# Kernel tuning notes

Hardware: AMD Instinct MI355X
Metric: run time of the kernel (lower is better)

## Reference

```python
import jax, jax.numpy as jnp
import numpy as np

UNITS = 128
D_FEAT = 128
B, N = 4, 4096
EDGE_PROB = 0.01  # avg in-degree ~ N * EDGE_PROB ~ 41


def setup_inputs() -> dict:
    key = jax.random.key(0)
    k1, k2, k3, k4 = jax.random.split(key, 4)
    x = jax.random.normal(k1, (B, N, D_FEAT), dtype=jnp.float32)
    # binary adjacency mask, as consumed by tf.where(adj)
    adj = (jax.random.uniform(k2, (B, N, N)) < EDGE_PROB).astype(jnp.float32)
    # Dense(units, use_bias=False) kernels: msg on concat(x_snd, x_rec) -> [2d, U];
    # node_update on concat(x, messages) -> [d+U, U]
    W_msg = (jax.random.normal(k3, (2 * D_FEAT, UNITS), dtype=jnp.float32)
             / np.sqrt(2 * D_FEAT).astype(np.float32))
    W_upd = (jax.random.normal(k4, (D_FEAT + UNITS, UNITS), dtype=jnp.float32)
             / np.sqrt(D_FEAT + UNITS).astype(np.float32))
    return {"x": x, "adj": adj, "W_msg": W_msg, "W_upd": W_upd}


def reference(x, adj, W_msg, W_upd):
    # Faithful to MPNN2.call: edges are (b, s, r) where adj[b, s, r] != 0.
    # message per edge = concat(x[b,s], x[b,r]) @ W_msg = x[b,s]@Ws + x[b,r]@Wr.
    # messages[b,r] = segment_mean over incoming edges. Since the receiver term
    # x[b,r]@Wr is identical for all edges into r, its mean is itself, and the
    # sender term's mean is (adj^T @ (x@Ws)) / in_degree. Empty segments -> 0
    # (tf.math.unsorted_segment_mean semantics). This avoids data-dependent
    # edge-list shapes and is jit-compatible.
    d = x.shape[-1]
    Ws, Wr = W_msg[:d], W_msg[d:]          # [d, U] each
    xs = x @ Ws                            # sender contribution  [B, N, U]
    xr = x @ Wr                            # receiver contribution [B, N, U]
    deg = jnp.einsum('bsr->br', adj)[..., None]          # in-degree [B, N, 1]
    snd_sum = jnp.einsum('bsr,bsu->bru', adj, xs)        # [B, N, U]
    messages = jnp.where(deg > 0,
                         snd_sum / jnp.maximum(deg, 1.0) + xr,
                         0.0)
    # node_update on concat(x, messages); activation=None, use_bias=False
    return jnp.concatenate([x, messages], axis=-1) @ W_upd
```

## Files before the change

kernel.cpp:

```cpp
#include <hip/hip_runtime.h>
#include <hip/hip_bf16.h>

#define BB 4
#define NN 4096
#define ROWS (BB*NN)
#define RT 128
#define SC 512
#define NCH (NN/SC)
#define CAPC 32
#define BSTRIDE (NCH*CAPC)

typedef __attribute__((ext_vector_type(8))) short short8;
typedef __attribute__((ext_vector_type(4))) float f32x4;

__device__ __forceinline__ float asf(unsigned int u) {
    union { unsigned int i; float f; } cv; cv.i = u; return cv.f;
}
__device__ __forceinline__ unsigned short f2bf(float f) {
    union { float f; unsigned int i; } cv; cv.f = f;
    unsigned int i = cv.i;
    return (unsigned short)((i + 0x7FFFu + ((i >> 16) & 1u)) >> 16);
}

__global__ __launch_bounds__(256) void scan_bucket(const float* __restrict__ adj,
                                                   int* __restrict__ cnt2,
                                                   int* __restrict__ bucket) {
    __shared__ int lcnt[RT];
    int bI = blockIdx.x;
    int rt = bI & 31;
    int ch = (bI >> 5) & 7;
    int b  = bI >> 8;
    int r0 = rt * RT;
    int s0 = ch * SC;
    int t  = threadIdx.x;
    if (t < RT) lcnt[t] = 0;
    __syncthreads();
    int cg = t & 31;
    int sl = t >> 5;
    const float* base = adj + ((size_t)b * NN + s0) * NN + r0 + cg * 4;
    for (int k = 0; k < SC / 32; ++k) {
        float4 v[4];
#pragma unroll
        for (int u = 0; u < 4; ++u)
            v[u] = *(const float4*)(base + (size_t)(k * 32 + u * 8 + sl) * NN);
#pragma unroll
        for (int u = 0; u < 4; ++u) {
            int s = s0 + k * 32 + u * 8 + sl;
            float vals[4] = {v[u].x, v[u].y, v[u].z, v[u].w};
#pragma unroll
            for (int j = 0; j < 4; ++j) {
                if (vals[j] != 0.0f) {
                    int col = cg * 4 + j;
                    int slot = atomicAdd(&lcnt[col], 1);
                    if (slot < CAPC)
                        bucket[(size_t)((b << 12) + r0 + col) * BSTRIDE + ch * CAPC + slot] = s;
                }
            }
        }
    }
    __syncthreads();
    if (t < RT) cnt2[(size_t)((b << 12) + r0 + t) * NCH + ch] = lcnt[t];
}

__global__ __launch_bounds__(128) void fold_weights(const float* __restrict__ Wmsg,
                                                    const float* __restrict__ Wupd,
                                                    unsigned short* __restrict__ WcatT) {
    __shared__ float ldsS[128], ldsR[128];
    int k = blockIdx.x, t = threadIdx.x;
    ldsS[t] = Wmsg[k * 128 + t];
    ldsR[t] = Wmsg[(128 + k) * 128 + t];
    __syncthreads();
    float a1 = 0.f, a2 = 0.f;
#pragma unroll 8
    for (int m = 0; m < 128; ++m) {
        float wu = Wupd[(128 + m) * 128 + t];
        a1 += ldsS[m] * wu;
        a2 += ldsR[m] * wu;
    }
    WcatT[(size_t)t * 128 + k]         = f2bf(Wupd[k * 128 + t]);
    WcatT[(size_t)(128 + t) * 128 + k] = f2bf(a2);
    WcatT[(size_t)(256 + t) * 128 + k] = f2bf(a1);
}

__global__ __launch_bounds__(256) void gemm_mfma(const float* __restrict__ X,
                                                 const unsigned short* __restrict__ WcatT,
                                                 float* __restrict__ TD,
                                                 unsigned short* __restrict__ YB) {
    __shared__ unsigned short Al[64][136];
    __shared__ unsigned short Bl[128][136];
    int t  = threadIdx.x;
    int m0 = blockIdx.x * 64;
    int nb = blockIdx.y;

    {
        int m = t >> 2, seg = t & 3;
        const float* src = X + (size_t)(m0 + m) * 128 + seg * 32;
#pragma unroll
        for (int i = 0; i < 8; ++i) {
            float4 v = *(const float4*)(src + i * 4);
            ushort4 p;
            p.x = f2bf(v.x); p.y = f2bf(v.y); p.z = f2bf(v.z); p.w = f2bf(v.w);
            *(ushort4*)&Al[m][seg * 32 + i * 4] = p;
        }
    }
    {
        int n = t >> 1, half = t & 1;
        const unsigned short* src = WcatT + (size_t)(nb * 128 + n) * 128 + half * 64;
#pragma unroll
        for (int i = 0; i < 8; ++i) {
            uint4 v = *(const uint4*)(src + i * 8);
            *(uint4*)&Bl[n][half * 64 + i * 8] = v;
        }
    }
    __syncthreads();

    int lane = t & 63, wave = t >> 6;
    int quad = lane >> 4, lr = lane & 15;
    int wm = wave * 16;
    f32x4 acc[8];
#pragma unroll
    for (int s = 0; s < 8; ++s) acc[s] = (f32x4)0.f;

#pragma unroll
    for (int kk = 0; kk < 4; ++kk) {
        short8 a = *(short8*)&Al[wm + lr][kk * 32 + quad * 8];
#pragma unroll
        for (int s = 0; s < 8; ++s) {
            short8 bf = *(short8*)&Bl[s * 16 + lr][kk * 32 + quad * 8];
            acc[s] = __builtin_amdgcn_mfma_f32_16x16x32_bf16(a, bf, acc[s], 0, 0, 0);
        }
    }

    if (nb == 2) {
#pragma unroll
        for (int s = 0; s < 8; ++s)
#pragma unroll
            for (int r = 0; r < 4; ++r) {
                int row = m0 + wm + quad * 4 + r;
                YB[(size_t)row * 128 + s * 16 + lr] = f2bf(acc[s][r]);
            }
    } else {
#pragma unroll
        for (int s = 0; s < 8; ++s)
#pragma unroll
            for (int r = 0; r < 4; ++r) {
                int row = m0 + wm + quad * 4 + r;
                TD[(size_t)row * 256 + nb * 128 + s * 16 + lr] = acc[s][r];
            }
    }
}

__global__ __launch_bounds__(256) void gather_out(const float* __restrict__ TD,
                                                  const unsigned int* __restrict__ YB,
                                                  const int* __restrict__ cnt2,
                                                  const int* __restrict__ bucket,
                                                  float* __restrict__ out) {
    __shared__ int lds_s[4][BSTRIDE];
    int t  = threadIdx.x;
    int rs = t >> 6;
    int j2 = t & 63;
    int rg = blockIdx.x * 4 + rs;

    int c[NCH];
    int ctot = 0, deg = 0;
    int pre[NCH];
#pragma unroll
    for (int ch = 0; ch < NCH; ++ch) {
        c[ch] = cnt2[(size_t)rg * NCH + ch];
        deg += c[ch];
        int cc = min(c[ch], CAPC);
        pre[ch] = ctot;
        ctot += cc;
    }
#pragma unroll
    for (int ch = 0; ch < NCH; ++ch) {
        int cc = min(c[ch], CAPC);
        if (j2 < cc)
            lds_s[rs][pre[ch] + j2] = bucket[(size_t)rg * BSTRIDE + ch * CAPC + j2];
    }
    __syncthreads();

    const float2* td = (const float2*)(TD + (size_t)rg * 256);
    float2 t1 = td[j2];
    float2 res = t1;
    if (deg > 0) {
        int b = rg >> 12;
        const unsigned int* yb = YB + (((size_t)b << 12)) * 64 + j2;
        float al0 = 0.f, ah0 = 0.f, al1 = 0.f, ah1 = 0.f;
        float al2 = 0.f, ah2 = 0.f, al3 = 0.f, ah3 = 0.f;
        int e = 0;
        for (; e + 4 <= ctot; e += 4) {
            int s0 = lds_s[rs][e + 0];
            int s1 = lds_s[rs][e + 1];
            int s2 = lds_s[rs][e + 2];
            int s3 = lds_s[rs][e + 3];
            unsigned u0 = yb[(size_t)s0 * 64];
            unsigned u1 = yb[(size_t)s1 * 64];
            unsigned u2 = yb[(size_t)s2 * 64];
            unsigned u3 = yb[(size_t)s3 * 64];
            al0 += asf(u0 << 16); ah0 += asf(u0 & 0xffff0000u);
            al1 += asf(u1 << 16); ah1 += asf(u1 & 0xffff0000u);
            al2 += asf(u2 << 16); ah2 += asf(u2 & 0xffff0000u);
            al3 += asf(u3 << 16); ah3 += asf(u3 & 0xffff0000u);
        }
        for (; e < ctot; ++e) {
            unsigned u = yb[(size_t)lds_s[rs][e] * 64];
            al0 += asf(u << 16); ah0 += asf(u & 0xffff0000u);
        }
        float inv = 1.0f / (float)deg;
        float2 d2 = td[64 + j2];
        res.x = t1.x + d2.x + (al0 + al1 + al2 + al3) * inv;
        res.y = t1.y + d2.y + (ah0 + ah1 + ah2 + ah3) * inv;
    }
    ((float2*)(out + (size_t)rg * 128))[j2] = res;
}

extern "C" void kernel_launch(void* const* d_in, const int* in_sizes, int n_in,
                              void* d_out, int out_size, void* d_ws, size_t ws_size,
                              hipStream_t stream) {
    const float* x    = (const float*)d_in[0];
    const float* adj  = (const float*)d_in[1];
    const float* Wmsg = (const float*)d_in[2];
    const float* Wupd = (const float*)d_in[3];
    float* out = (float*)d_out;

    char* ws = (char*)d_ws;
    unsigned short* WcatT  = (unsigned short*)(ws);
    float*          TD     = (float*)(ws + 131072);
    unsigned short* YB     = (unsigned short*)(ws + 131072 + 16777216);
    int*            cnt2   = (int*)(ws + 131072 + 16777216 + 4194304);
    int*            bucket = (int*)(ws + 131072 + 16777216 + 4194304 + 524288);

    scan_bucket<<<1024, 256, 0, stream>>>(adj, cnt2, bucket);
    fold_weights<<<128, 128, 0, stream>>>(Wmsg, Wupd, WcatT);
    gemm_mfma<<<dim3(256, 3), 256, 0, stream>>>(x, WcatT, TD, YB);
    gather_out<<<ROWS / 4, 256, 0, stream>>>(TD, (const unsigned int*)YB, cnt2, bucket, out);
}
```

Measured before the change: 433.2 us.

## Replace sparse bucket scan and gather with dense bf16 MFMA SpMM over adjacency

```diff
diff --git a/kernel.cpp b/kernel.cpp
--- a/kernel.cpp
+++ b/kernel.cpp
@@ -4,62 +4,14 @@
 #define BB 4
 #define NN 4096
 #define ROWS (BB*NN)
-#define RT 128
-#define SC 512
-#define NCH (NN/SC)
-#define CAPC 32
-#define BSTRIDE (NCH*CAPC)
 
 typedef __attribute__((ext_vector_type(8))) short short8;
 typedef __attribute__((ext_vector_type(4))) float f32x4;
 
-__device__ __forceinline__ float asf(unsigned int u) {
-    union { unsigned int i; float f; } cv; cv.i = u; return cv.f;
-}
 __device__ __forceinline__ unsigned short f2bf(float f) {
     union { float f; unsigned int i; } cv; cv.f = f;
     unsigned int i = cv.i;
     return (unsigned short)((i + 0x7FFFu + ((i >> 16) & 1u)) >> 16);
-}
-
-__global__ __launch_bounds__(256) void scan_bucket(const float* __restrict__ adj,
-                                                   int* __restrict__ cnt2,
-                                                   int* __restrict__ bucket) {
-    __shared__ int lcnt[RT];
-    int bI = blockIdx.x;
-    int rt = bI & 31;
-    int ch = (bI >> 5) & 7;
-    int b  = bI >> 8;
-    int r0 = rt * RT;
-    int s0 = ch * SC;
-    int t  = threadIdx.x;
-    if (t < RT) lcnt[t] = 0;
-    __syncthreads();
-    int cg = t & 31;
-    int sl = t >> 5;
-    const float* base = adj + ((size_t)b * NN + s0) * NN + r0 + cg * 4;
-    for (int k = 0; k < SC / 32; ++k) {
-        float4 v[4];
-#pragma unroll
-        for (int u = 0; u < 4; ++u)
-            v[u] = *(const float4*)(base + (size_t)(k * 32 + u * 8 + sl) * NN);
-#pragma unroll
-        for (int u = 0; u < 4; ++u) {
-            int s = s0 + k * 32 + u * 8 + sl;
-            float vals[4] = {v[u].x, v[u].y, v[u].z, v[u].w};
-#pragma unroll
-            for (int j = 0; j < 4; ++j) {
-                if (vals[j] != 0.0f) {
-                    int col = cg * 4 + j;
-                    int slot = atomicAdd(&lcnt[col], 1);
-                    if (slot < CAPC)
-                        bucket[(size_t)((b << 12) + r0 + col) * BSTRIDE + ch * CAPC + slot] = s;
-                }
-            }
-        }
-    }
-    __syncthreads();
-    if (t < RT) cnt2[(size_t)((b << 12) + r0 + t) * NCH + ch] = lcnt[t];
 }
 
 __global__ __launch_bounds__(128) void fold_weights(const float* __restrict__ Wmsg,
@@ -85,7 +37,7 @@
 __global__ __launch_bounds__(256) void gemm_mfma(const float* __restrict__ X,
                                                  const unsigned short* __restrict__ WcatT,
                                                  float* __restrict__ TD,
-                                                 unsigned short* __restrict__ YB) {
+                                                 unsigned short* __restrict__ YT) {
     __shared__ unsigned short Al[64][136];
     __shared__ unsigned short Bl[128][136];
     int t  = threadIdx.x;
@@ -132,13 +84,16 @@
     }
 
     if (nb == 2) {
-#pragma unroll
-        for (int s = 0; s < 8; ++s)
-#pragma unroll
-            for (int r = 0; r < 4; ++r) {
-                int row = m0 + wm + quad * 4 + r;
-                YB[(size_t)row * 128 + s * 16 + lr] = f2bf(acc[s][r]);
-            }
+        int row0 = m0 + wm + quad * 4;
+        int b = row0 >> 12, s0 = row0 & 4095;
+#pragma unroll
+        for (int s = 0; s < 8; ++s) {
+            int u = s * 16 + lr;
+            ushort4 pk;
+            pk.x = f2bf(acc[s][0]); pk.y = f2bf(acc[s][1]);
+            pk.z = f2bf(acc[s][2]); pk.w = f2bf(acc[s][3]);
+            *(ushort4*)(&YT[((size_t)b * 128 + u) * 4096 + s0]) = pk;
+        }
     } else {
 #pragma unroll
         for (int s = 0; s < 8; ++s)
@@ -150,69 +105,86 @@
     }
 }
 
-__global__ __launch_bounds__(256) void gather_out(const float* __restrict__ TD,
-                                                  const unsigned int* __restrict__ YB,
-                                                  const int* __restrict__ cnt2,
-                                                  const int* __restrict__ bucket,
-                                                  float* __restrict__ out) {
-    __shared__ int lds_s[4][BSTRIDE];
-    int t  = threadIdx.x;
-    int rs = t >> 6;
-    int j2 = t & 63;
-    int rg = blockIdx.x * 4 + rs;
-
-    int c[NCH];
-    int ctot = 0, deg = 0;
-    int pre[NCH];
-#pragma unroll
-    for (int ch = 0; ch < NCH; ++ch) {
-        c[ch] = cnt2[(size_t)rg * NCH + ch];
-        deg += c[ch];
-        int cc = min(c[ch], CAPC);
-        pre[ch] = ctot;
-        ctot += cc;
-    }
-#pragma unroll
-    for (int ch = 0; ch < NCH; ++ch) {
-        int cc = min(c[ch], CAPC);
-        if (j2 < cc)
-            lds_s[rs][pre[ch] + j2] = bucket[(size_t)rg * BSTRIDE + ch * CAPC + j2];
-    }
-    __syncthreads();
-
-    const float2* td = (const float2*)(TD + (size_t)rg * 256);
-    float2 t1 = td[j2];
-    float2 res = t1;
-    if (deg > 0) {
-        int b = rg >> 12;
-        const unsigned int* yb = YB + (((size_t)b << 12)) * 64 + j2;
-        float al0 = 0.f, ah0 = 0.f, al1 = 0.f, ah1 = 0.f;
-        float al2 = 0.f, ah2 = 0.f, al3 = 0.f, ah3 = 0.f;
-        int e = 0;
-        for (; e + 4 <= ctot; e += 4) {
-            int s0 = lds_s[rs][e + 0];
-            int s1 = lds_s[rs][e + 1];
-            int s2 = lds_s[rs][e + 2];
-            int s3 = lds_s[rs][e + 3];
-            unsigned u0 = yb[(size_t)s0 * 64];
-            unsigned u1 = yb[(size_t)s1 * 64];
-            unsigned u2 = yb[(size_t)s2 * 64];
-            unsigned u3 = yb[(size_t)s3 * 64];
-            al0 += asf(u0 << 16); ah0 += asf(u0 & 0xffff0000u);
-            al1 += asf(u1 << 16); ah1 += asf(u1 & 0xffff0000u);
-            al2 += asf(u2 << 16); ah2 += asf(u2 & 0xffff0000u);
-            al3 += asf(u3 << 16); ah3 += asf(u3 & 0xffff0000u);
-        }
-        for (; e < ctot; ++e) {
-            unsigned u = yb[(size_t)lds_s[rs][e] * 64];
-            al0 += asf(u << 16); ah0 += asf(u & 0xffff0000u);
-        }
-        float inv = 1.0f / (float)deg;
-        float2 d2 = td[64 + j2];
-        res.x = t1.x + d2.x + (al0 + al1 + al2 + al3) * inv;
-        res.y = t1.y + d2.y + (ah0 + ah1 + ah2 + ah3) * inv;
-    }
-    ((float2*)(out + (size_t)rg * 128))[j2] = res;
+__global__ __launch_bounds__(512) void spmm_mfma(const float* __restrict__ adj,
+                                                 const unsigned short* __restrict__ YT,
+                                                 const float* __restrict__ TD,
+                                                 float* __restrict__ out) {
+    int bI = blockIdx.x;
+    int b  = (bI & 7) >> 1;
+    int mt = ((bI >> 3) << 1) | (bI & 1);
+    int r0 = mt * 64;
+
+    int t = threadIdx.x;
+    int w = t >> 6;
+    int wm = w >> 1;
+    int wn = w & 1;
+    int lane = t & 63;
+    int quad = lane >> 4, lr = lane & 15;
+    int rbase = r0 + wm * 16;
+
+    const float* ap = adj + ((size_t)b << 24) + ((size_t)(quad * 8) << 12) + rbase + lr;
+    const unsigned short* yp = YT + ((size_t)b * 128 + wn * 64 + lr) * 4096 + quad * 8;
+
+    f32x4 acc[4];
+#pragma unroll
+    for (int i = 0; i < 4; ++i) acc[i] = (f32x4)0.f;
+    float degp = 0.f;
+
+    float fa[8]; short8 bv[4];
+#pragma unroll
+    for (int j = 0; j < 8; ++j) fa[j] = ap[(size_t)j << 12];
+#pragma unroll
+    for (int n = 0; n < 4; ++n) bv[n] = *(const short8*)(yp + ((size_t)n << 16));
+
+#pragma unroll 2
+    for (int c = 0; c < 128; ++c) {
+        float fn[8]; short8 bn[4];
+        if (c < 127) {
+            size_t soff = (size_t)((c + 1) * 32) << 12;
+#pragma unroll
+            for (int j = 0; j < 8; ++j) fn[j] = ap[soff + ((size_t)j << 12)];
+            int yoff = (c + 1) * 32;
+#pragma unroll
+            for (int n = 0; n < 4; ++n) bn[n] = *(const short8*)(yp + ((size_t)n << 16) + yoff);
+        }
+        short8 av;
+#pragma unroll
+        for (int j = 0; j < 8; ++j) {
+            degp += fa[j];
+            union { float f; unsigned int i; } cv; cv.f = fa[j];
+            av[j] = (short)(cv.i >> 16);
+        }
+#pragma unroll
+        for (int n = 0; n < 4; ++n)
+            acc[n] = __builtin_amdgcn_mfma_f32_16x16x32_bf16(av, bv[n], acc[n], 0, 0, 0);
+#pragma unroll
+        for (int j = 0; j < 8; ++j) fa[j] = fn[j];
+#pragma unroll
+        for (int n = 0; n < 4; ++n) bv[n] = bn[n];
+    }
+
+    degp += __shfl_xor(degp, 16, 64);
+    degp += __shfl_xor(degp, 32, 64);
+    float degm[4], invd[4];
+#pragma unroll
+    for (int r = 0; r < 4; ++r) {
+        degm[r] = __shfl(degp, quad * 4 + r, 64);
+        invd[r] = degm[r] > 0.f ? 1.0f / degm[r] : 0.f;
+    }
+
+    int rgbase = (b << 12) + rbase + quad * 4;
+#pragma unroll
+    for (int n = 0; n < 4; ++n) {
+        int u = (wn * 4 + n) * 16 + lr;
+#pragma unroll
+        for (int r = 0; r < 4; ++r) {
+            int row = rgbase + r;
+            float t1 = TD[(size_t)row * 256 + u];
+            float d2 = TD[(size_t)row * 256 + 128 + u];
+            float res = t1 + (degm[r] > 0.f ? d2 + acc[n][r] * invd[r] : 0.f);
+            out[(size_t)row * 128 + u] = res;
+        }
+    }
 }
 
 extern "C" void kernel_launch(void* const* d_in, const int* in_sizes, int n_in,
@@ -225,14 +197,11 @@
     float* out = (float*)d_out;
 
     char* ws = (char*)d_ws;
-    unsigned short* WcatT  = (unsigned short*)(ws);
-    float*          TD     = (float*)(ws + 131072);
-    unsigned short* YB     = (unsigned short*)(ws + 131072 + 16777216);
-    int*            cnt2   = (int*)(ws + 131072 + 16777216 + 4194304);
-    int*            bucket = (int*)(ws + 131072 + 16777216 + 4194304 + 524288);
-
-    scan_bucket<<<1024, 256, 0, stream>>>(adj, cnt2, bucket);
+    unsigned short* WcatT = (unsigned short*)(ws);
+    float*          TD    = (float*)(ws + 131072);
+    unsigned short* YT    = (unsigned short*)(ws + 131072 + 16777216);
+
     fold_weights<<<128, 128, 0, stream>>>(Wmsg, Wupd, WcatT);
-    gemm_mfma<<<dim3(256, 3), 256, 0, stream>>>(x, WcatT, TD, YB);
-    gather_out<<<ROWS / 4, 256, 0, stream>>>(TD, (const unsigned int*)YB, cnt2, bucket, out);
-}
+    gemm_mfma<<<dim3(ROWS / 64, 3), 256, 0, stream>>>(x, WcatT, TD, YT);
+    spmm_mfma<<<256, 512, 0, stream>>>(adj, YT, TD, out);
+}
```

Measured after the change: 503.4 us. 1.16x slower.

## Restructure adjacency scan to per-thread columns without shared atomics, wave-scan gather

Applied to the files above, without the earlier changes.

```diff
diff --git a/kernel.cpp b/kernel.cpp
--- a/kernel.cpp
+++ b/kernel.cpp
@@ -4,10 +4,9 @@
 #define BB 4
 #define NN 4096
 #define ROWS (BB*NN)
-#define RT 128
-#define SC 512
-#define NCH (NN/SC)
-#define CAPC 32
+#define SROWS 64
+#define NCH (NN/SROWS)
+#define CAPC 12
 #define BSTRIDE (NCH*CAPC)
 
 typedef __attribute__((ext_vector_type(8))) short short8;
@@ -22,44 +21,46 @@
     return (unsigned short)((i + 0x7FFFu + ((i >> 16) & 1u)) >> 16);
 }
 
-__global__ __launch_bounds__(256) void scan_bucket(const float* __restrict__ adj,
-                                                   int* __restrict__ cnt2,
-                                                   int* __restrict__ bucket) {
-    __shared__ int lcnt[RT];
+__global__ __launch_bounds__(1024) void scan_bucket(const float* __restrict__ adj,
+                                                    int* __restrict__ cnt2,
+                                                    int* __restrict__ bucket) {
     int bI = blockIdx.x;
-    int rt = bI & 31;
-    int ch = (bI >> 5) & 7;
-    int b  = bI >> 8;
-    int r0 = rt * RT;
-    int s0 = ch * SC;
+    int ch = bI & (NCH - 1);
+    int b  = bI >> 6;
+    int s0 = ch * SROWS;
     int t  = threadIdx.x;
-    if (t < RT) lcnt[t] = 0;
-    __syncthreads();
-    int cg = t & 31;
-    int sl = t >> 5;
-    const float* base = adj + ((size_t)b * NN + s0) * NN + r0 + cg * 4;
-    for (int k = 0; k < SC / 32; ++k) {
-        float4 v[4];
-#pragma unroll
-        for (int u = 0; u < 4; ++u)
-            v[u] = *(const float4*)(base + (size_t)(k * 32 + u * 8 + sl) * NN);
-#pragma unroll
-        for (int u = 0; u < 4; ++u) {
-            int s = s0 + k * 32 + u * 8 + sl;
-            float vals[4] = {v[u].x, v[u].y, v[u].z, v[u].w};
+    int c0 = t << 2;
+
+    const float* base = adj + ((size_t)b * NN + s0) * NN + c0;
+    int* bp[4];
+#pragma unroll
+    for (int j = 0; j < 4; ++j)
+        bp[j] = bucket + (size_t)((b << 12) + c0 + j) * BSTRIDE + ch * CAPC;
+
+    int cnt[4] = {0, 0, 0, 0};
+
+    uint4 v = *(const uint4*)(base);
+#pragma unroll 2
+    for (int it = 0; it < SROWS; ++it) {
+        uint4 vn;
+        if (it < SROWS - 1)
+            vn = *(const uint4*)(base + (size_t)(it + 1) * NN);
+        if ((v.x | v.y | v.z | v.w) != 0u) {
+            int s = s0 + it;
+            unsigned uv[4] = {v.x, v.y, v.z, v.w};
 #pragma unroll
             for (int j = 0; j < 4; ++j) {
-                if (vals[j] != 0.0f) {
-                    int col = cg * 4 + j;
-                    int slot = atomicAdd(&lcnt[col], 1);
-                    if (slot < CAPC)
-                        bucket[(size_t)((b << 12) + r0 + col) * BSTRIDE + ch * CAPC + slot] = s;
+                if (uv[j] != 0u) {
+                    int slot = cnt[j]++;
+                    if (slot < CAPC) bp[j][slot] = s;
                 }
             }
         }
-    }
-    __syncthreads();
-    if (t < RT) cnt2[(size_t)((b << 12) + r0 + t) * NCH + ch] = lcnt[t];
+        v = vn;
+    }
+#pragma unroll
+    for (int j = 0; j < 4; ++j)
+        cnt2[(size_t)((b << 12) + c0 + j) * NCH + ch] = cnt[j];
 }
 
 __global__ __launch_bounds__(128) void fold_weights(const float* __restrict__ Wmsg,
@@ -161,22 +162,28 @@
     int j2 = t & 63;
     int rg = blockIdx.x * 4 + rs;
 
-    int c[NCH];
-    int ctot = 0, deg = 0;
-    int pre[NCH];
-#pragma unroll
+    int c  = cnt2[(size_t)rg * NCH + j2];
+    int cc = min(c, CAPC);
+
+    int deg = c;
+#pragma unroll
+    for (int d = 1; d < 64; d <<= 1) deg += __shfl_xor(deg, d, 64);
+
+    int incl = cc;
+#pragma unroll
+    for (int d = 1; d < 64; d <<= 1) {
+        int n = __shfl_up(incl, d, 64);
+        if (j2 >= d) incl += n;
+    }
+    int pre  = incl - cc;
+    int ctot = __shfl(incl, 63, 64);
+
     for (int ch = 0; ch < NCH; ++ch) {
-        c[ch] = cnt2[(size_t)rg * NCH + ch];
-        deg += c[ch];
-        int cc = min(c[ch], CAPC);
-        pre[ch] = ctot;
-        ctot += cc;
-    }
-#pragma unroll
-    for (int ch = 0; ch < NCH; ++ch) {
-        int cc = min(c[ch], CAPC);
-        if (j2 < cc)
-            lds_s[rs][pre[ch] + j2] = bucket[(size_t)rg * BSTRIDE + ch * CAPC + j2];
+        int cc_ch = __shfl(cc, ch, 64);
+        if (cc_ch == 0) continue;
+        int pre_ch = __shfl(pre, ch, 64);
+        if (j2 < cc_ch)
+            lds_s[rs][pre_ch + j2] = bucket[(size_t)rg * BSTRIDE + ch * CAPC + j2];
     }
     __syncthreads();
 
@@ -229,10 +236,10 @@
     float*          TD     = (float*)(ws + 131072);
     unsigned short* YB     = (unsigned short*)(ws + 131072 + 16777216);
     int*            cnt2   = (int*)(ws + 131072 + 16777216 + 4194304);
-    int*            bucket = (int*)(ws + 131072 + 16777216 + 4194304 + 524288);
-
-    scan_bucket<<<1024, 256, 0, stream>>>(adj, cnt2, bucket);
+    int*            bucket = (int*)(ws + 131072 + 16777216 + 4194304 + 4194304);
+
+    scan_bucket<<<BB * NCH, 1024, 0, stream>>>(adj, cnt2, bucket);
     fold_weights<<<128, 128, 0, stream>>>(Wmsg, Wupd, WcatT);
-    gemm_mfma<<<dim3(256, 3), 256, 0, stream>>>(x, WcatT, TD, YB);
+    gemm_mfma<<<dim3(ROWS / 64, 3), 256, 0, stream>>>(x, WcatT, TD, YB);
     gather_out<<<ROWS / 4, 256, 0, stream>>>(TD, (const unsigned int*)YB, cnt2, bucket, out);
 }
```

Measured after the change: 489.6 us. +13.0%, slower.
